# Performance work log

Hardware: AMD Instinct MI355X
Metric: run time of the kernel (lower is better)

The kernel has to match this reference:

```python
import jax, jax.numpy as jnp
import numpy as np

# ---- static config (decode path of PagedAttention) ----
B = 16            # batch (one new token per sequence in decode)
H = 32            # query heads
KVH = 8           # kv heads (GQA)
G = H // KVH      # query heads per kv head group
D = 128           # head dim (Rope hard-codes split at 64)
BLOCK = 16        # block_size hard-coded in forward
CACHE_LEN = 4096  # cache_length[b] for every b (uniform)
NUM_FETCH = CACHE_LEN // BLOCK          # 256 full blocks fetched per seq
MAX_BLOCKS = B * (NUM_FETCH + 1)        # 4112; one spare block per seq
ROWS = MAX_BLOCKS * BLOCK               # 65792 flat cache rows
SCALE = 1.0 / np.sqrt(D)                # softmax_scale


def setup_inputs() -> dict:
    key = jax.random.key(0)
    ks = jax.random.split(key, 6)
    Q = jax.random.normal(ks[0], (B, H, D), jnp.float32)
    K = jax.random.normal(ks[1], (B, KVH, D), jnp.float32)
    V = jax.random.normal(ks[2], (B, KVH, D), jnp.float32)
    Kcache = jax.random.normal(ks[3], (ROWS, KVH, D), jnp.float32)
    Vcache = jax.random.normal(ks[4], (ROWS, KVH, D), jnp.float32)
    # rotary cos/sin for the current decode position (one per sequence)
    inv_freq = 1.0 / (10000.0 ** (jnp.arange(D // 2, dtype=jnp.float32) / (D // 2)))
    pos = jnp.full((B, 1), float(CACHE_LEN), dtype=jnp.float32)
    ang = pos * inv_freq[None, :]                      # [B, 64]
    cos = jnp.concatenate([jnp.cos(ang), jnp.cos(ang)], axis=-1)  # [B, 128]
    sin = jnp.concatenate([jnp.sin(ang), jnp.sin(ang)], axis=-1)
    # block-aligned page table: seq b owns blocks [b*257, b*257+256)
    fetch_slots = ((jnp.arange(B, dtype=jnp.int32)[:, None] * (NUM_FETCH + 1)
                    + jnp.arange(NUM_FETCH, dtype=jnp.int32)[None, :]) * BLOCK)
    save_slots = ((jnp.arange(B, dtype=jnp.int32) * (NUM_FETCH + 1) + NUM_FETCH)
                  * BLOCK).reshape(B, 1)
    return dict(Q=Q, K=K, V=V, Kcache=Kcache, Vcache=Vcache,
                cos=cos, sin=sin, fetch_slots=fetch_slots, save_slots=save_slots)


def _rope(x, cos, sin):
    # x: [B, heads, 128]; matches torch: x*cos + concat(-x2, x1)*sin
    x1, x2 = x[..., :D // 2], x[..., D // 2:]
    rot = jnp.concatenate([-x2, x1], axis=-1)
    return x * cos[:, None, :] + rot * sin[:, None, :]


def reference(Q, K, V, Kcache, Vcache, cos, sin, fetch_slots, save_slots):
    Qr = _rope(Q, cos, sin)          # [B, H, D]
    Kr = _rope(K, cos, sin)          # [B, KVH, D]
    # cache physical per-block layout is [kv_heads, block, d]
    Kc4 = Kcache.reshape(MAX_BLOCKS, KVH, BLOCK, D)
    Vc4 = Vcache.reshape(MAX_BLOCKS, KVH, BLOCK, D)
    blk = fetch_slots // BLOCK                         # [B, NUM_FETCH]
    # paged gather: [B, NF, KVH, BLOCK, D] -> [B, KVH, CACHE_LEN, D]
    Kb = jnp.transpose(Kc4[blk], (0, 2, 1, 3, 4)).reshape(B, KVH, CACHE_LEN, D)
    Vb = jnp.transpose(Vc4[blk], (0, 2, 1, 3, 4)).reshape(B, KVH, CACHE_LEN, D)
    # append the new (roped) K and raw V token -> N = CACHE_LEN + 1
    Kall = jnp.concatenate([Kb, Kr[:, :, None, :]], axis=2)
    Vall = jnp.concatenate([Vb, V[:, :, None, :]], axis=2)
    # torch's tile-repeat maps query head h -> kv head h % KVH;
    # reshape [B, G, KVH, D] puts head g*KVH+k at [g, k], kv index k. Exact match.
    Qg = Qr.reshape(B, G, KVH, D)
    scores = jnp.einsum('bgkd,bknd->bgkn', Qg, Kall) * SCALE   # [B,G,KVH,N]
    p = jax.nn.softmax(scores, axis=-1)
    Yg = jnp.einsum('bgkn,bknd->bgkd', p, Vall)                # [B,G,KVH,D]
    Y = Yg.reshape(B, H, D)
    # scatter-write of new K/V into save_slots (in-place cache update in torch;
    # does not affect Y since save blocks are disjoint from fetch blocks)
    # Kc4.at[save_slots[:,0]//BLOCK, :, save_slots[:,0]%BLOCK, :].set(Kr)
    return Y


if __name__ == '__main__':
    out = reference(**setup_inputs())
    print(out.shape, out.dtype)
```

## Files before the change

### kernel.cpp

```cpp
#include <hip/hip_runtime.h>

#define NB 16
#define NH 32
#define NKVH 8
#define NG 4
#define ND 128
#define BLOCK 16
#define NUM_FETCH 256
#define NSPLIT 32
#define PAGES_PER_WG 8
#define ITERS 4

static constexpr float SCALE_LOG2E = 0.08838834764831845f * 1.4426950408889634f;


__global__ __launch_bounds__(256, 4) void pa_main(
    const float* __restrict__ Q,
    const float* __restrict__ Kcache,
    const float* __restrict__ Vcache,
    const float* __restrict__ cosb,
    const float* __restrict__ sinb,
    const int*   __restrict__ fetch,
    float* __restrict__ accws,
    float* __restrict__ lws)
{
    const int wg    = blockIdx.x;
    const int split = wg & (NSPLIT - 1);
    const int kvh   = (wg >> 5) & (NKVH - 1);
    const int b     = wg >> 8;

    const int tid  = threadIdx.x;
    const int w    = tid >> 6;
    const int lane = tid & 63;
    const int half = lane >> 5;
    const int l32  = lane & 31;
    const int d0   = l32 << 2;

    const int* fb = fetch + b * NUM_FETCH + split * PAGES_PER_WG;
    const int  ps = w >> 1;
    const int  r0 = ((w & 1) * 2 + half) * 4;

    const float4 cs = *(const float4*)(cosb + b * ND + d0);
    const float4 sn = *(const float4*)(sinb + b * ND + d0);
    const float  sgn = (d0 < 64) ? -1.f : 1.f;
    const int    dp  = d0 ^ 64;
    float qv[NG][4];
    #pragma unroll
    for (int g = 0; g < NG; ++g) {
        const float* qp = Q + (size_t)(b * NH + g * NKVH + kvh) * ND;
        const float4 qa = *(const float4*)(qp + d0);
        const float4 qb = *(const float4*)(qp + dp);
        qv[g][0] = (qa.x * cs.x + sgn * qb.x * sn.x) * SCALE_LOG2E;
        qv[g][1] = (qa.y * cs.y + sgn * qb.y * sn.y) * SCALE_LOG2E;
        qv[g][2] = (qa.z * cs.z + sgn * qb.z * sn.z) * SCALE_LOG2E;
        qv[g][3] = (qa.w * cs.w + sgn * qb.w * sn.w) * SCALE_LOG2E;
    }

    float acc[NG][4] = {{0.f,0.f,0.f,0.f},{0.f,0.f,0.f,0.f},
                        {0.f,0.f,0.f,0.f},{0.f,0.f,0.f,0.f}};
    float lsum[NG] = {0.f, 0.f, 0.f, 0.f};

    const size_t gbase = (size_t)kvh * (BLOCK * ND) + (size_t)r0 * ND + d0;
    const float* kb = Kcache + gbase;
    const float* vb = Vcache + gbase;

    int pgNext = fb[ps];

    #pragma unroll 1
    for (int i = 0; i < ITERS; ++i) {
        const int pg = __builtin_amdgcn_readfirstlane(pgNext);
        const int ni = (i + 1 < ITERS) ? (i + 1) * 2 + ps : ps;
        pgNext = fb[ni];

        const size_t off = (size_t)pg * (NKVH * ND);
        const float4 k0 = *(const float4*)(kb + off);
        const float4 k1 = *(const float4*)(kb + off + 1 * ND);
        const float4 k2 = *(const float4*)(kb + off + 2 * ND);
        const float4 k3 = *(const float4*)(kb + off + 3 * ND);
        const float4 v0 = *(const float4*)(vb + off);
        const float4 v1 = *(const float4*)(vb + off + 1 * ND);
        const float4 v2 = *(const float4*)(vb + off + 2 * ND);
        const float4 v3 = *(const float4*)(vb + off + 3 * ND);

        float s[4][NG];
        #pragma unroll
        for (int g = 0; g < NG; ++g) {
            s[0][g] = qv[g][0]*k0.x + qv[g][1]*k0.y + qv[g][2]*k0.z + qv[g][3]*k0.w;
            s[1][g] = qv[g][0]*k1.x + qv[g][1]*k1.y + qv[g][2]*k1.z + qv[g][3]*k1.w;
            s[2][g] = qv[g][0]*k2.x + qv[g][1]*k2.y + qv[g][2]*k2.z + qv[g][3]*k2.w;
            s[3][g] = qv[g][0]*k3.x + qv[g][1]*k3.y + qv[g][2]*k3.z + qv[g][3]*k3.w;
        }

        #pragma unroll
        for (int m = 16; m >= 1; m >>= 1) {
            #pragma unroll
            for (int r = 0; r < 4; ++r)
                #pragma unroll
                for (int g = 0; g < NG; ++g)
                    s[r][g] += __shfl_xor(s[r][g], m, 64);
        }

        #pragma unroll
        for (int g = 0; g < NG; ++g) {
            const float p0 = __builtin_amdgcn_exp2f(s[0][g]);
            const float p1 = __builtin_amdgcn_exp2f(s[1][g]);
            const float p2 = __builtin_amdgcn_exp2f(s[2][g]);
            const float p3 = __builtin_amdgcn_exp2f(s[3][g]);
            lsum[g] += (p0 + p1) + (p2 + p3);
            acc[g][0] += p0 * v0.x + p1 * v1.x + p2 * v2.x + p3 * v3.x;
            acc[g][1] += p0 * v0.y + p1 * v1.y + p2 * v2.y + p3 * v3.y;
            acc[g][2] += p0 * v0.z + p1 * v1.z + p2 * v2.z + p3 * v3.z;
            acc[g][3] += p0 * v0.w + p1 * v1.w + p2 * v2.w + p3 * v3.w;
        }
    }

    #pragma unroll
    for (int g = 0; g < NG; ++g) {
        lsum[g] += __shfl_xor(lsum[g], 32, 64);
        #pragma unroll
        for (int j = 0; j < 4; ++j)
            acc[g][j] += __shfl_xor(acc[g][j], 32, 64);
    }

    __shared__ float s_acc[4][NG][ND];
    __shared__ float s_l[4][NG];
    if (half == 0) {
        #pragma unroll
        for (int g = 0; g < NG; ++g)
            *(float4*)&s_acc[w][g][d0] =
                make_float4(acc[g][0], acc[g][1], acc[g][2], acc[g][3]);
        if (l32 == 0) {
            #pragma unroll
            for (int g = 0; g < NG; ++g) s_l[w][g] = lsum[g];
        }
    }
    __syncthreads();

    const size_t pslot = (size_t)(b * NKVH + kvh) * NSPLIT + split;
    for (int idx = tid; idx < NG * ND; idx += 256) {
        const int g = idx >> 7, d = idx & 127;
        accws[(pslot * NG + g) * ND + d] =
            s_acc[0][g][d] + s_acc[1][g][d] + s_acc[2][g][d] + s_acc[3][g][d];
    }
    if (tid < NG)
        lws[pslot * NG + tid] = s_l[0][tid] + s_l[1][tid] + s_l[2][tid] + s_l[3][tid];
}

__global__ __launch_bounds__(128) void pa_combine(
    const float* __restrict__ Q,
    const float* __restrict__ Knew,
    const float* __restrict__ Vnew,
    const float* __restrict__ cosb,
    const float* __restrict__ sinb,
    const float* __restrict__ accws,
    const float* __restrict__ lws,
    float* __restrict__ Y)
{
    const int bh  = blockIdx.x;
    const int b   = bh >> 5;
    const int h   = bh & (NH - 1);
    const int kvh = h & (NKVH - 1);
    const int g   = h >> 3;
    const int d   = threadIdx.x;

    const float c   = cosb[b * ND + d];
    const float s   = sinb[b * ND + d];
    const float sgn = (d < 64) ? -1.f : 1.f;
    const int   dp  = d ^ 64;
    const float* qp = Q    + (size_t)(b * NH + h) * ND;
    const float* kp = Knew + (size_t)(b * NKVH + kvh) * ND;
    const float qr = qp[d] * c + sgn * qp[dp] * s;
    const float kr = kp[d] * c + sgn * kp[dp] * s;

    float prod = qr * kr;
    #pragma unroll
    for (int m = 32; m >= 1; m >>= 1) prod += __shfl_xor(prod, m, 64);
    __shared__ float red[2];
    if ((d & 63) == 0) red[d >> 6] = prod;
    __syncthreads();

    const float p = __builtin_amdgcn_exp2f((red[0] + red[1]) * SCALE_LOG2E);

    const size_t base = ((size_t)(b * NKVH + kvh) * NSPLIT) * NG + g;
    float acc = p * Vnew[(size_t)(b * NKVH + kvh) * ND + d];
    float lt  = p;
    #pragma unroll
    for (int sp = 0; sp < NSPLIT; ++sp) {
        acc += accws[(base + (size_t)sp * NG) * ND + d];
        lt  += lws[base + (size_t)sp * NG];
    }
    Y[(size_t)(b * NH + h) * ND + d] = acc / lt;
}

extern "C" void kernel_launch(void* const* d_in, const int* in_sizes, int n_in,
                              void* d_out, int out_size, void* d_ws, size_t ws_size,
                              hipStream_t stream)
{
    const float* Q    = (const float*)d_in[0];
    const float* K    = (const float*)d_in[1];
    const float* V    = (const float*)d_in[2];
    const float* Kc   = (const float*)d_in[3];
    const float* Vc   = (const float*)d_in[4];
    const float* cosb = (const float*)d_in[5];
    const float* sinb = (const float*)d_in[6];
    const int*   fetch = (const int*)d_in[7];

    float* accws = (float*)d_ws;
    float* lws   = accws + (size_t)NB * NKVH * NSPLIT * NG * ND;
    float* Y     = (float*)d_out;

    pa_main<<<NB * NKVH * NSPLIT, 256, 0, stream>>>(Q, Kc, Vc, cosb, sinb, fetch, accws, lws);
    pa_combine<<<NB * NH, 128, 0, stream>>>(Q, K, V, cosb, sinb, accws, lws, Y);
}
```

Before: 118.3 us.

## Double-buffer K/V page loads and halve split count with longer per-workgroup loops

Halves the number of splits per (batch, kv-head) so each workgroup handles twice as many pages. The page loop is fully unrolled with register double-buffering, so the next page's K/V loads are issued before the current page's compute, and a sched_barrier keeps the compiler from reordering them. Page indices are all read up front via readfirstlane. This aims to hide memory latency and cut combine work, at the cost of more registers (launch bounds lowered to 3 waves) and fewer workgroups in flight.

```diff
diff --git a/kernel.cpp b/kernel.cpp
--- a/kernel.cpp
+++ b/kernel.cpp
@@ -7,14 +7,13 @@
 #define ND 128
 #define BLOCK 16
 #define NUM_FETCH 256
-#define NSPLIT 32
-#define PAGES_PER_WG 8
-#define ITERS 4
+#define NSPLIT 16
+#define PAGES_PER_WG 16
+#define ITERS 8
 
 static constexpr float SCALE_LOG2E = 0.08838834764831845f * 1.4426950408889634f;
 
-
-__global__ __launch_bounds__(256, 4) void pa_main(
+__global__ __launch_bounds__(256, 3) void pa_main(
     const float* __restrict__ Q,
     const float* __restrict__ Kcache,
     const float* __restrict__ Vcache,
@@ -26,8 +25,8 @@
 {
     const int wg    = blockIdx.x;
     const int split = wg & (NSPLIT - 1);
-    const int kvh   = (wg >> 5) & (NKVH - 1);
-    const int b     = wg >> 8;
+    const int kvh   = (wg >> 4) & (NKVH - 1);
+    const int b     = wg >> 7;
 
     const int tid  = threadIdx.x;
     const int w    = tid >> 6;
@@ -39,6 +38,11 @@
     const int* fb = fetch + b * NUM_FETCH + split * PAGES_PER_WG;
     const int  ps = w >> 1;
     const int  r0 = ((w & 1) * 2 + half) * 4;
+
+    int pgv[ITERS];
+    #pragma unroll
+    for (int i = 0; i < ITERS; ++i)
+        pgv[i] = __builtin_amdgcn_readfirstlane(fb[2 * i + ps]);
 
     const float4 cs = *(const float4*)(cosb + b * ND + d0);
     const float4 sn = *(const float4*)(sinb + b * ND + d0);
@@ -64,42 +68,32 @@
     const float* kb = Kcache + gbase;
     const float* vb = Vcache + gbase;
 
-    int pgNext = fb[ps];
-
-    #pragma unroll 1
-    for (int i = 0; i < ITERS; ++i) {
-        const int pg = __builtin_amdgcn_readfirstlane(pgNext);
-        const int ni = (i + 1 < ITERS) ? (i + 1) * 2 + ps : ps;
-        pgNext = fb[ni];
-
+    float4 kA[4], vA[4], kB[4], vB[4];
+
+    auto load_set = [&](float4 (&K4)[4], float4 (&V4)[4], int pg) {
         const size_t off = (size_t)pg * (NKVH * ND);
-        const float4 k0 = *(const float4*)(kb + off);
-        const float4 k1 = *(const float4*)(kb + off + 1 * ND);
-        const float4 k2 = *(const float4*)(kb + off + 2 * ND);
-        const float4 k3 = *(const float4*)(kb + off + 3 * ND);
-        const float4 v0 = *(const float4*)(vb + off);
-        const float4 v1 = *(const float4*)(vb + off + 1 * ND);
-        const float4 v2 = *(const float4*)(vb + off + 2 * ND);
-        const float4 v3 = *(const float4*)(vb + off + 3 * ND);
-
+        #pragma unroll
+        for (int r = 0; r < 4; ++r) {
+            K4[r] = *(const float4*)(kb + off + (size_t)r * ND);
+            V4[r] = *(const float4*)(vb + off + (size_t)r * ND);
+        }
+    };
+
+    auto body = [&](const float4 (&K4)[4], const float4 (&V4)[4]) {
         float s[4][NG];
         #pragma unroll
-        for (int g = 0; g < NG; ++g) {
-            s[0][g] = qv[g][0]*k0.x + qv[g][1]*k0.y + qv[g][2]*k0.z + qv[g][3]*k0.w;
-            s[1][g] = qv[g][0]*k1.x + qv[g][1]*k1.y + qv[g][2]*k1.z + qv[g][3]*k1.w;
-            s[2][g] = qv[g][0]*k2.x + qv[g][1]*k2.y + qv[g][2]*k2.z + qv[g][3]*k2.w;
-            s[3][g] = qv[g][0]*k3.x + qv[g][1]*k3.y + qv[g][2]*k3.z + qv[g][3]*k3.w;
-        }
-
-        #pragma unroll
-        for (int m = 16; m >= 1; m >>= 1) {
+        for (int r = 0; r < 4; ++r)
+            #pragma unroll
+            for (int g = 0; g < NG; ++g)
+                s[r][g] = qv[g][0]*K4[r].x + qv[g][1]*K4[r].y
+                        + qv[g][2]*K4[r].z + qv[g][3]*K4[r].w;
+        #pragma unroll
+        for (int m = 16; m >= 1; m >>= 1)
             #pragma unroll
             for (int r = 0; r < 4; ++r)
                 #pragma unroll
                 for (int g = 0; g < NG; ++g)
                     s[r][g] += __shfl_xor(s[r][g], m, 64);
-        }
-
         #pragma unroll
         for (int g = 0; g < NG; ++g) {
             const float p0 = __builtin_amdgcn_exp2f(s[0][g]);
@@ -107,11 +101,25 @@
             const float p2 = __builtin_amdgcn_exp2f(s[2][g]);
             const float p3 = __builtin_amdgcn_exp2f(s[3][g]);
             lsum[g] += (p0 + p1) + (p2 + p3);
-            acc[g][0] += p0 * v0.x + p1 * v1.x + p2 * v2.x + p3 * v3.x;
-            acc[g][1] += p0 * v0.y + p1 * v1.y + p2 * v2.y + p3 * v3.y;
-            acc[g][2] += p0 * v0.z + p1 * v1.z + p2 * v2.z + p3 * v3.z;
-            acc[g][3] += p0 * v0.w + p1 * v1.w + p2 * v2.w + p3 * v3.w;
-        }
+            acc[g][0] += p0 * V4[0].x + p1 * V4[1].x + p2 * V4[2].x + p3 * V4[3].x;
+            acc[g][1] += p0 * V4[0].y + p1 * V4[1].y + p2 * V4[2].y + p3 * V4[3].y;
+            acc[g][2] += p0 * V4[0].z + p1 * V4[1].z + p2 * V4[2].z + p3 * V4[3].z;
+            acc[g][3] += p0 * V4[0].w + p1 * V4[1].w + p2 * V4[2].w + p3 * V4[3].w;
+        }
+    };
+
+    load_set(kA, vA, pgv[0]);
+
+    #pragma unroll
+    for (int i = 0; i < ITERS; ++i) {
+        const bool curA = (i & 1) == 0;
+        if (i + 1 < ITERS) {
+            if (curA) load_set(kB, vB, pgv[i + 1]);
+            else      load_set(kA, vA, pgv[i + 1]);
+            __builtin_amdgcn_sched_barrier(0);
+        }
+        if (curA) body(kA, vA);
+        else      body(kB, vB);
     }
 
     #pragma unroll
```

Measured after the change: 456.0 us. +285.5%, slower.

## Stage paged K/V through LDS with async global_load_lds double buffering

Applied to the files above, without the earlier changes.

The main kernel now has each wave load its own four pages of K and V into LDS using direct global-to-LDS loads. It double-buffers 8-row pieces and waits on vmcnt so the next piece streams in while the current one is computed. The split count is halved so each workgroup covers 16 pages, which halves the partial-result workspace traffic and the combine loop length. The costs are 64KB of LDS per workgroup, which limits occupancy, fewer workgroups in flight, and hand-written waitcnt sequencing that could break correctness if the compiler reorders memory operations.

```diff
diff --git a/kernel.cpp b/kernel.cpp
--- a/kernel.cpp
+++ b/kernel.cpp
@@ -7,14 +7,24 @@
 #define ND 128
 #define BLOCK 16
 #define NUM_FETCH 256
-#define NSPLIT 32
-#define PAGES_PER_WG 8
-#define ITERS 4
+#define NSPLIT 16
+#define PAGES_PER_WG 16
+#define PAGES_PER_WAVE 4
+#define PIECES 8
+#define PIECE_ROWS 8
+#define PIECE_FLOATS (PIECE_ROWS * ND)
 
 static constexpr float SCALE_LOG2E = 0.08838834764831845f * 1.4426950408889634f;
 
 
-__global__ __launch_bounds__(256, 4) void pa_main(
+__device__ __forceinline__ void gld_lds16(const float* g, float* l) {
+    __builtin_amdgcn_global_load_lds(
+        (const __attribute__((address_space(1))) void*)g,
+        (__attribute__((address_space(3))) void*)l,
+        16, 0, 0);
+}
+
+__global__ __launch_bounds__(256) void pa_main(
     const float* __restrict__ Q,
     const float* __restrict__ Kcache,
     const float* __restrict__ Vcache,
@@ -26,8 +36,8 @@
 {
     const int wg    = blockIdx.x;
     const int split = wg & (NSPLIT - 1);
-    const int kvh   = (wg >> 5) & (NKVH - 1);
-    const int b     = wg >> 8;
+    const int kvh   = (wg >> 4) & (NKVH - 1);
+    const int b     = wg >> 7;
 
     const int tid  = threadIdx.x;
     const int w    = tid >> 6;
@@ -37,8 +47,28 @@
     const int d0   = l32 << 2;
 
     const int* fb = fetch + b * NUM_FETCH + split * PAGES_PER_WG;
-    const int  ps = w >> 1;
-    const int  r0 = ((w & 1) * 2 + half) * 4;
+
+    int pgv[PAGES_PER_WAVE];
+    #pragma unroll
+    for (int i = 0; i < PAGES_PER_WAVE; ++i)
+        pgv[i] = __builtin_amdgcn_readfirstlane(fb[w * PAGES_PER_WAVE + i]);
+
+    __shared__ float kbuf[4][2][PIECE_FLOATS];
+    __shared__ float vbuf[4][2][PIECE_FLOATS];
+
+    const size_t khead = (size_t)kvh * (BLOCK * ND);
+
+    auto stage = [&](int s, int p) {
+        const size_t base = (size_t)pgv[p >> 1] * (NKVH * ND) + khead
+                          + (size_t)(p & 1) * PIECE_FLOATS;
+        const float* kg = Kcache + base + lane * 4;
+        const float* vg = Vcache + base + lane * 4;
+        #pragma unroll
+        for (int i = 0; i < 4; ++i) {
+            gld_lds16(kg + i * 256, &kbuf[w][s][i * 256]);
+            gld_lds16(vg + i * 256, &vbuf[w][s][i * 256]);
+        }
+    };
 
     const float4 cs = *(const float4*)(cosb + b * ND + d0);
     const float4 sn = *(const float4*)(sinb + b * ND + d0);
@@ -60,58 +90,59 @@
                         {0.f,0.f,0.f,0.f},{0.f,0.f,0.f,0.f}};
     float lsum[NG] = {0.f, 0.f, 0.f, 0.f};
 
-    const size_t gbase = (size_t)kvh * (BLOCK * ND) + (size_t)r0 * ND + d0;
-    const float* kb = Kcache + gbase;
-    const float* vb = Vcache + gbase;
-
-    int pgNext = fb[ps];
-
-    #pragma unroll 1
-    for (int i = 0; i < ITERS; ++i) {
-        const int pg = __builtin_amdgcn_readfirstlane(pgNext);
-        const int ni = (i + 1 < ITERS) ? (i + 1) * 2 + ps : ps;
-        pgNext = fb[ni];
-
-        const size_t off = (size_t)pg * (NKVH * ND);
-        const float4 k0 = *(const float4*)(kb + off);
-        const float4 k1 = *(const float4*)(kb + off + 1 * ND);
-        const float4 k2 = *(const float4*)(kb + off + 2 * ND);
-        const float4 k3 = *(const float4*)(kb + off + 3 * ND);
-        const float4 v0 = *(const float4*)(vb + off);
-        const float4 v1 = *(const float4*)(vb + off + 1 * ND);
-        const float4 v2 = *(const float4*)(vb + off + 2 * ND);
-        const float4 v3 = *(const float4*)(vb + off + 3 * ND);
-
-        float s[4][NG];
-        #pragma unroll
-        for (int g = 0; g < NG; ++g) {
-            s[0][g] = qv[g][0]*k0.x + qv[g][1]*k0.y + qv[g][2]*k0.z + qv[g][3]*k0.w;
-            s[1][g] = qv[g][0]*k1.x + qv[g][1]*k1.y + qv[g][2]*k1.z + qv[g][3]*k1.w;
-            s[2][g] = qv[g][0]*k2.x + qv[g][1]*k2.y + qv[g][2]*k2.z + qv[g][3]*k2.w;
-            s[3][g] = qv[g][0]*k3.x + qv[g][1]*k3.y + qv[g][2]*k3.z + qv[g][3]*k3.w;
+    stage(0, 0);
+    stage(1, 1);
+
+    #pragma unroll
+    for (int j = 0; j < PIECES; ++j) {
+        if (j < PIECES - 1) asm volatile("s_waitcnt vmcnt(8)" ::: "memory");
+        else                asm volatile("s_waitcnt vmcnt(0)" ::: "memory");
+        __builtin_amdgcn_sched_barrier(0);
+
+        {
+            const float* kp = &kbuf[w][j & 1][half * 4 * ND + d0];
+            const float* vp = &vbuf[w][j & 1][half * 4 * ND + d0];
+            const float4 k0 = *(const float4*)(kp);
+            const float4 k1 = *(const float4*)(kp + ND);
+            const float4 k2 = *(const float4*)(kp + 2 * ND);
+            const float4 k3 = *(const float4*)(kp + 3 * ND);
+            const float4 v0 = *(const float4*)(vp);
+            const float4 v1 = *(const float4*)(vp + ND);
+            const float4 v2 = *(const float4*)(vp + 2 * ND);
+            const float4 v3 = *(const float4*)(vp + 3 * ND);
+
+            float s[4][NG];
+            #pragma unroll
+            for (int g = 0; g < NG; ++g) {
+                s[0][g] = qv[g][0]*k0.x + qv[g][1]*k0.y + qv[g][2]*k0.z + qv[g][3]*k0.w;
+                s[1][g] = qv[g][0]*k1.x + qv[g][1]*k1.y + qv[g][2]*k1.z + qv[g][3]*k1.w;
+                s[2][g] = qv[g][0]*k2.x + qv[g][1]*k2.y + qv[g][2]*k2.z + qv[g][3]*k2.w;
+                s[3][g] = qv[g][0]*k3.x + qv[g][1]*k3.y + qv[g][2]*k3.z + qv[g][3]*k3.w;
+            }
+            #pragma unroll
+            for (int m = 16; m >= 1; m >>= 1)
+                #pragma unroll
+                for (int r = 0; r < 4; ++r)
+                    #pragma unroll
+                    for (int g = 0; g < NG; ++g)
+                        s[r][g] += __shfl_xor(s[r][g], m, 64);
+            #pragma unroll
+            for (int g = 0; g < NG; ++g) {
+                const float p0 = __builtin_amdgcn_exp2f(s[0][g]);
+                const float p1 = __builtin_amdgcn_exp2f(s[1][g]);
+                const float p2 = __builtin_amdgcn_exp2f(s[2][g]);
+                const float p3 = __builtin_amdgcn_exp2f(s[3][g]);
+                lsum[g] += (p0 + p1) + (p2 + p3);
+                acc[g][0] += p0 * v0.x + p1 * v1.x + p2 * v2.x + p3 * v3.x;
+                acc[g][1] += p0 * v0.y + p1 * v1.y + p2 * v2.y + p3 * v3.y;
+                acc[g][2] += p0 * v0.z + p1 * v1.z + p2 * v2.z + p3 * v3.z;
+                acc[g][3] += p0 * v0.w + p1 * v1.w + p2 * v2.w + p3 * v3.w;
+            }
         }
 
-        #pragma unroll
-        for (int m = 16; m >= 1; m >>= 1) {
-            #pragma unroll
-            for (int r = 0; r < 4; ++r)
-                #pragma unroll
-                for (int g = 0; g < NG; ++g)
-                    s[r][g] += __shfl_xor(s[r][g], m, 64);
-        }
-
-        #pragma unroll
-        for (int g = 0; g < NG; ++g) {
-            const float p0 = __builtin_amdgcn_exp2f(s[0][g]);
-            const float p1 = __builtin_amdgcn_exp2f(s[1][g]);
-            const float p2 = __builtin_amdgcn_exp2f(s[2][g]);
-            const float p3 = __builtin_amdgcn_exp2f(s[3][g]);
-            lsum[g] += (p0 + p1) + (p2 + p3);
-            acc[g][0] += p0 * v0.x + p1 * v1.x + p2 * v2.x + p3 * v3.x;
-            acc[g][1] += p0 * v0.y + p1 * v1.y + p2 * v2.y + p3 * v3.y;
-            acc[g][2] += p0 * v0.z + p1 * v1.z + p2 * v2.z + p3 * v3.z;
-            acc[g][3] += p0 * v0.w + p1 * v1.w + p2 * v2.w + p3 * v3.w;
-        }
+        asm volatile("s_waitcnt lgkmcnt(0)" ::: "memory");
+        __builtin_amdgcn_sched_barrier(0);
+        if (j + 2 < PIECES) stage(j & 1, j + 2);
     }
 
     #pragma unroll
@@ -122,16 +153,17 @@
             acc[g][j] += __shfl_xor(acc[g][j], 32, 64);
     }
 
-    __shared__ float s_acc[4][NG][ND];
-    __shared__ float s_l[4][NG];
+    __syncthreads();
+    float* s_acc = &kbuf[0][0][0];
+    float* s_l   = &vbuf[0][0][0];
     if (half == 0) {
         #pragma unroll
         for (int g = 0; g < NG; ++g)
-            *(float4*)&s_acc[w][g][d0] =
+            *(float4*)&s_acc[(w * NG + g) * ND + d0] =
                 make_float4(acc[g][0], acc[g][1], acc[g][2], acc[g][3]);
         if (l32 == 0) {
             #pragma unroll
-            for (int g = 0; g < NG; ++g) s_l[w][g] = lsum[g];
+            for (int g = 0; g < NG; ++g) s_l[w * NG + g] = lsum[g];
         }
     }
     __syncthreads();
@@ -140,10 +172,12 @@
     for (int idx = tid; idx < NG * ND; idx += 256) {
         const int g = idx >> 7, d = idx & 127;
         accws[(pslot * NG + g) * ND + d] =
-            s_acc[0][g][d] + s_acc[1][g][d] + s_acc[2][g][d] + s_acc[3][g][d];
+            s_acc[(0 * NG + g) * ND + d] + s_acc[(1 * NG + g) * ND + d] +
+            s_acc[(2 * NG + g) * ND + d] + s_acc[(3 * NG + g) * ND + d];
     }
     if (tid < NG)
-        lws[pslot * NG + tid] = s_l[0][tid] + s_l[1][tid] + s_l[2][tid] + s_l[3][tid];
+        lws[pslot * NG + tid] = s_l[0 * NG + tid] + s_l[1 * NG + tid]
+                              + s_l[2 * NG + tid] + s_l[3 * NG + tid];
 }
 
 __global__ __launch_bounds__(128) void pa_combine(
```

Result: slower. 164.7 us (+39.2%).
